# Kernel optimization log

Measured on AMD Instinct MI355X. Metric: run time of the kernel, lower is better.

## Reference

```python
import jax, jax.numpy as jnp
import numpy as np

N_NODES = 100000
N_EDGES = 1000000
IN_FEATS = 128
HID_FEATS = 128
OUT_FEATS = 128
N_CLASSES = 16
NEG_SLOPE = 0.01
BN_EPS = 1e-5


def _linear_params(key, d_in, d_out):
    k1, k2 = jax.random.split(key)
    s = 1.0 / np.sqrt(d_in)
    w = jax.random.uniform(k1, (d_in, d_out), jnp.float32, -s, s)
    b = jax.random.uniform(k2, (d_out,), jnp.float32, -s, s)
    return w, b


def setup_inputs() -> dict:
    key = jax.random.key(0)
    ks = jax.random.split(key, 16)
    node_feat = jax.random.normal(ks[0], (N_NODES, IN_FEATS), jnp.float32)
    src = jax.random.randint(ks[1], (N_EDGES,), 0, N_NODES, jnp.int32)
    dst = jax.random.randint(ks[2], (N_EDGES,), 0, N_NODES, jnp.int32)
    dims = [(IN_FEATS, HID_FEATS), (HID_FEATS, HID_FEATS), (HID_FEATS, OUT_FEATS)]
    inp = {"node_feat": node_feat, "src": src, "dst": dst}
    for i, (din, dout) in enumerate(dims):
        wp, bp = _linear_params(ks[3 + 4 * i], din, din)      # fc_pool: d_in -> d_in
        ws, _ = _linear_params(ks[4 + 4 * i], din, dout)       # fc_self (no bias)
        wn, _ = _linear_params(ks[5 + 4 * i], din, dout)       # fc_neigh (no bias)
        _, b = _linear_params(ks[6 + 4 * i], din, dout)        # shared output bias
        inp[f"wp{i}"] = wp; inp[f"bp{i}"] = bp
        inp[f"ws{i}"] = ws; inp[f"wn{i}"] = wn; inp[f"b{i}"] = b
    inp["bn_gamma"] = jnp.ones((HID_FEATS,), jnp.float32)
    inp["bn_beta"] = jnp.zeros((HID_FEATS,), jnp.float32)
    wc, bc = _linear_params(ks[15], OUT_FEATS, N_CLASSES)
    inp["wc"] = wc; inp["bc"] = bc
    return inp


def _sage_pool(h, src, dst, deg_mask, wp, bp, ws, wn, b):
    # fc_pool + relu on source nodes, gather per edge, segment-max to dst
    hp = jax.nn.relu(h @ wp + bp)                 # [N, d_in]
    msg = hp[src]                                 # [E, d_in]
    agg = jax.ops.segment_max(msg, dst, num_segments=N_NODES)  # [N, d_in]
    agg = jnp.where(deg_mask, agg, 0.0)           # zero for isolated nodes
    return h @ ws + agg @ wn + b


def _batchnorm(x, gamma, beta):
    mu = jnp.mean(x, axis=0)
    var = jnp.var(x, axis=0)
    return (x - mu) * jax.lax.rsqrt(var + BN_EPS) * gamma + beta


def reference(node_feat, src, dst,
              wp0, bp0, ws0, wn0, b0,
              wp1, bp1, ws1, wn1, b1,
              wp2, bp2, ws2, wn2, b2,
              bn_gamma, bn_beta, wc, bc):
    deg = jnp.zeros((N_NODES,), jnp.float32).at[dst].add(1.0)
    deg_mask = (deg > 0)[:, None]
    h = jax.nn.leaky_relu(_sage_pool(node_feat, src, dst, deg_mask, wp0, bp0, ws0, wn0, b0), NEG_SLOPE)
    h = jax.nn.leaky_relu(_batchnorm(_sage_pool(h, src, dst, deg_mask, wp1, bp1, ws1, wn1, b1), bn_gamma, bn_beta), NEG_SLOPE)
    h = _sage_pool(h, src, dst, deg_mask, wp2, bp2, ws2, wn2, b2)
    return h @ wc + bc
```

## Files before the change

### kernel.cpp

```cpp
#include <hip/hip_runtime.h>


#define N_NODES 100000
#define N_EDGES 1000000
#define F 128
#define NEG_SLOPE 0.01f
#define BN_EPS 1e-5f
#define NODES_PER_XCD 12500

typedef __attribute__((ext_vector_type(8))) short bf16x8;
typedef __attribute__((ext_vector_type(4))) float f32x4;
typedef __attribute__((ext_vector_type(2))) unsigned short u16x2;

typedef __attribute__((address_space(3))) unsigned int as3_uint;
typedef __attribute__((address_space(1))) const unsigned int as1_cuint;

__device__ __forceinline__ void gload16(const void* g, void* l) {
    __builtin_amdgcn_global_load_lds((as1_cuint*)g, (as3_uint*)l, 16, 0, 0);
}

__device__ __forceinline__ unsigned short f2bf(float f) {
    unsigned int u = __float_as_uint(f);
    u += 0x7fff + ((u >> 16) & 1);
    return (unsigned short)(u >> 16);
}
__device__ __forceinline__ float bf2f(unsigned short h) {
    return __uint_as_float(((unsigned int)h) << 16);
}

__global__ __launch_bounds__(256) void zero_misc_kernel(
    float4* __restrict__ deg4, float4* __restrict__ stats4)
{
    if (blockIdx.x < 98) {
        const int i = blockIdx.x * 256 + threadIdx.x;
        if (i < 25000) deg4[i] = make_float4(0.f, 0.f, 0.f, 0.f);
    } else {
        if (threadIdx.x < 64) stats4[threadIdx.x] = make_float4(0.f, 0.f, 0.f, 0.f);
    }
}

#define PREP_GROUPS 4483
__global__ __launch_bounds__(256) void prep_kernel(
    const float4* __restrict__ nf, uint2* __restrict__ xout,
    const int* __restrict__ dst, int* __restrict__ deg,
    const float* __restrict__ w0, const float* __restrict__ w1, const float* __restrict__ w2,
    const float* __restrict__ w3, const float* __restrict__ w4, const float* __restrict__ w5,
    const float* __restrict__ w6, const float* __restrict__ w7, const float* __restrict__ w8,
    short* __restrict__ wp_p, short* __restrict__ wsn_p)
{
    const int g = blockIdx.x >> 2;
    const int k = blockIdx.x & 3;
    const int tid = threadIdx.x;
    if (k < 3) {
        const int c = g * 3 + k;
        if (c >= 12500) return;
        const long i = (long)c * 256 + tid;
        float4 v = nf[i];
        uint2 o;
        o.x = (unsigned)f2bf(v.x) | ((unsigned)f2bf(v.y) << 16);
        o.y = (unsigned)f2bf(v.z) | ((unsigned)f2bf(v.w) << 16);
        xout[i] = o;
        return;
    }
    if (g < 3907) {
        const int e = g * 256 + tid;
        if (e < N_EDGES) atomicAdd(&deg[__builtin_nontemporal_load(&dst[e])], 1);
        return;
    }
    const int po = g - 3907;
    if (po >= 576) return;
    const int idx = po * 256 + tid;
    const int matid = idx >> 14;
    const int layer = (matid * 11) >> 5;
    const int mat = matid - 3 * layer;
    const int i = idx & 16383;
    const int kk = i >> 7, n = i & 127;
    const float* srcm;
    switch (matid) {
        case 0: srcm = w0; break; case 1: srcm = w1; break; case 2: srcm = w2; break;
        case 3: srcm = w3; break; case 4: srcm = w4; break; case 5: srcm = w5; break;
        case 6: srcm = w6; break; case 7: srcm = w7; break; default: srcm = w8; break;
    }
    const int slot = ((kk >> 3) * 128 + n) * 8 + (kk & 7);
    const short v = (short)f2bf(srcm[i]);
    if (mat == 0) wp_p[layer * 16384 + slot] = v;
    else wsn_p[layer * 32768 + (mat == 2 ? 16384 : 0) + slot] = v;
}

template<int NKS>
__device__ __forceinline__ void gemm_body(
    const int bid,
    const short* __restrict__ A1, const short* __restrict__ A2,
    const short* __restrict__ Bp, const float* __restrict__ bias,
    unsigned short* __restrict__ Cout, const int n_rows, const int act)
{
    constexpr int S = NKS / 2;
    __shared__ short tile[2 * 8192];

    const int tid = threadIdx.x;
    const int wave = tid >> 6;
    const int lane = tid & 63;
    const int m = lane & 15, q = lane >> 4;
    const int r0 = bid * 128;
    const int rw = (wave >> 1) * 64;
    const int r0q = r0 + rw;
    const int c0 = (wave & 1) * 64;
    const int gchunk = (tid & 7) ^ ((tid >> 3) & 7);

    f32x4 acc[4][4];
#pragma unroll
    for (int i = 0; i < 4; ++i)
#pragma unroll
        for (int j = 0; j < 4; ++j)
#pragma unroll
            for (int r = 0; r < 4; ++r) acc[i][j][r] = 0.f;

    auto stage = [&](int s, int buf) {
        const short* Ap = (NKS == 8 && s >= 2) ? A2 : A1;
        const int kbase = (s & 1) * 64;
#pragma unroll
        for (int p = 0; p < 4; ++p) {
            int row = r0 + (tid >> 3) + 32 * p;
            row = min(row, n_rows - 1);
            gload16(Ap + (size_t)row * F + kbase + gchunk * 8,
                    &tile[buf * 8192 + p * 2048 + tid * 8]);
        }
    };

    stage(0, 0);
    __syncthreads();

    for (int s = 0; s < S; ++s) {
        if (s + 1 < S) stage(s + 1, (s + 1) & 1);
        const short* tb = &tile[(s & 1) * 8192];
#pragma unroll
        for (int ks2 = 0; ks2 < 2; ++ks2) {
            const int ks32 = s * 2 + ks2;
            bf16x8 b[4], a[4];
#pragma unroll
            for (int ni = 0; ni < 4; ++ni)
                b[ni] = *(const bf16x8*)(Bp + ((size_t)(ks32 * 4 + q) * F + c0 + ni * 16 + m) * 8);
#pragma unroll
            for (int mi = 0; mi < 4; ++mi)
                a[mi] = *(const bf16x8*)(tb + (rw + mi * 16 + m) * 64 + (((ks2 * 4 + q) ^ (m & 7)) << 3));
#pragma unroll
            for (int mi = 0; mi < 4; ++mi)
#pragma unroll
                for (int ni = 0; ni < 4; ++ni)
                    acc[mi][ni] = __builtin_amdgcn_mfma_f32_16x16x32_bf16(a[mi], b[ni], acc[mi][ni], 0, 0, 0);
        }
        __syncthreads();
    }

    float bv[4];
#pragma unroll
    for (int ni = 0; ni < 4; ++ni) bv[ni] = bias[c0 + ni * 16 + m];

    short* ep = &tile[wave * 1280];
    const int colc_lo = m >> 3, cin = m & 7;
#pragma unroll
    for (int mi = 0; mi < 4; ++mi) {
#pragma unroll
        for (int ni = 0; ni < 4; ++ni) {
            const int colc = 2 * ni + colc_lo;
#pragma unroll
            for (int rg = 0; rg < 4; ++rg) {
                const int row16 = q * 4 + rg;
                float v = acc[mi][ni][rg] + bv[ni];
                if (act == 1) v = v > 0.f ? v : 0.f;
                else if (act == 2) v = v > 0.f ? v : v * NEG_SLOPE;
                ep[row16 * 80 + ((colc ^ (row16 & 7)) << 3) + cin] = (short)f2bf(v);
            }
        }
        __syncthreads();
#pragma unroll
        for (int p = 0; p < 2; ++p) {
            const int lrow = (lane >> 3) + 8 * p;
            bf16x8 vv = *(const bf16x8*)&ep[lrow * 80 + (((lane & 7) ^ (lrow & 7)) << 3)];
            const int grow = r0q + mi * 16 + lrow;
            if (grow < n_rows)
                *(bf16x8*)(Cout + (size_t)grow * F + c0 + ((lane & 7) << 3)) = vv;
        }
        __syncthreads();
    }
}

template<int NKS>
__global__ __launch_bounds__(256) void gemm_mfma(
    const short* __restrict__ A1, const short* __restrict__ A2,
    const short* __restrict__ Bp, const float* __restrict__ bias,
    unsigned short* __restrict__ Cout, int n_rows, int act)
{
    gemm_body<NKS>(blockIdx.x, A1, A2, Bp, bias, Cout, n_rows, act);
}

template<int EPI>
__global__ __launch_bounds__(256) void gemm8_fused(
    const short* __restrict__ A1, const short* __restrict__ A2,
    const short* __restrict__ Bp, const float* __restrict__ bias,
    unsigned short* __restrict__ Cout,
    const short* __restrict__ Bp2, const float* __restrict__ bias2,
    unsigned short* __restrict__ Cout2,
    float* __restrict__ stats,
    const float* __restrict__ Wc, const float* __restrict__ bc,
    float* __restrict__ out,
    int n_rows, int act)
{
    __shared__ short tile[2 * 8192];
    __shared__ float wcS[EPI == 3 ? 2064 : 4];

    const int tid = threadIdx.x;
    const int wave = tid >> 6;
    const int lane = tid & 63;
    const int m = lane & 15, q = lane >> 4;
    const int r0 = blockIdx.x * 128;
    const int rw = (wave >> 1) * 64;
    const int r0q = r0 + rw;
    const int c0 = (wave & 1) * 64;
    const int gchunk = (tid & 7) ^ ((tid >> 3) & 7);

    if constexpr (EPI == 3) {
        for (int i = tid; i < 2048; i += 256) wcS[i] = Wc[i];
        if (tid < 16) wcS[2048 + tid] = bc[tid];
    }

    f32x4 acc[4][4];
#pragma unroll
    for (int i = 0; i < 4; ++i)
#pragma unroll
        for (int j = 0; j < 4; ++j)
#pragma unroll
            for (int r = 0; r < 4; ++r) acc[i][j][r] = 0.f;

    auto stage = [&](int s, int buf) {
        const short* Ap = (s >= 2) ? A2 : A1;
        const int kbase = (s & 1) * 64;
#pragma unroll
        for (int p = 0; p < 4; ++p) {
            int row = r0 + (tid >> 3) + 32 * p;
            row = min(row, n_rows - 1);
            gload16(Ap + (size_t)row * F + kbase + gchunk * 8,
                    &tile[buf * 8192 + p * 2048 + tid * 8]);
        }
    };

    auto compute_step = [&](const short* __restrict__ Bpp, int s, f32x4 (&ac)[4][4]) {
        const short* tb = &tile[(s & 1) * 8192];
#pragma unroll
        for (int ks2 = 0; ks2 < 2; ++ks2) {
            const int ks32 = s * 2 + ks2;
            bf16x8 b[4], a[4];
#pragma unroll
            for (int ni = 0; ni < 4; ++ni)
                b[ni] = *(const bf16x8*)(Bpp + ((size_t)(ks32 * 4 + q) * F + c0 + ni * 16 + m) * 8);
#pragma unroll
            for (int mi = 0; mi < 4; ++mi)
                a[mi] = *(const bf16x8*)(tb + (rw + mi * 16 + m) * 64 + (((ks2 * 4 + q) ^ (m & 7)) << 3));
#pragma unroll
            for (int mi = 0; mi < 4; ++mi)
#pragma unroll
                for (int ni = 0; ni < 4; ++ni)
                    ac[mi][ni] = __builtin_amdgcn_mfma_f32_16x16x32_bf16(a[mi], b[ni], ac[mi][ni], 0, 0, 0);
        }
    };

    stage(0, 0);
    __syncthreads();
    for (int s = 0; s < 4; ++s) {
        if (s + 1 < 4) stage(s + 1, (s + 1) & 1);
        compute_step(Bp, s, acc);
        __syncthreads();
    }

    float bv[4];
#pragma unroll
    for (int ni = 0; ni < 4; ++ni) bv[ni] = bias[c0 + ni * 16 + m];

    if constexpr (EPI == 1 || EPI == 3) {
        const int bufo = (wave & 1) * 8192;
#pragma unroll
        for (int mi = 0; mi < 4; ++mi)
#pragma unroll
            for (int ni = 0; ni < 4; ++ni) {
                const int chunk = ni * 2 + (m >> 3);
#pragma unroll
                for (int rg = 0; rg < 4; ++rg) {
                    const int r = rw + mi * 16 + q * 4 + rg;
                    float v = acc[mi][ni][rg] + bv[ni];
                    if (act == 1) v = v > 0.f ? v : 0.f;
                    else if (act == 2) v = v > 0.f ? v : v * NEG_SLOPE;
                    tile[bufo + r * 64 + ((chunk ^ (r & 7)) << 3) + (m & 7)] = (short)f2bf(v);
                }
            }
        __syncthreads();
    }

    if constexpr (EPI == 1) {
        {
            const int r = tid >> 1, half = tid & 1;
            const int grow = r0 + r;
            if (grow < n_rows) {
#pragma unroll
                for (int c = 0; c < 8; ++c) {
                    bf16x8 vv = *(const bf16x8*)&tile[half * 8192 + r * 64 + ((c ^ (r & 7)) << 3)];
                    *(bf16x8*)(Cout + (size_t)grow * F + half * 64 + c * 8) = vv;
                }
            }
        }
        f32x4 ac2[4][4];
#pragma unroll
        for (int i = 0; i < 4; ++i)
#pragma unroll
            for (int j = 0; j < 4; ++j)
#pragma unroll
                for (int r = 0; r < 4; ++r) ac2[i][j][r] = 0.f;
        compute_step(Bp2, 0, ac2);
        compute_step(Bp2, 1, ac2);
        __syncthreads();

        float bv2[4];
#pragma unroll
        for (int ni = 0; ni < 4; ++ni) bv2[ni] = bias2[c0 + ni * 16 + m];
        short* ep = &tile[wave * 1280];
        const int colc_lo = m >> 3, cin = m & 7;
#pragma unroll
        for (int mi = 0; mi < 4; ++mi) {
#pragma unroll
            for (int ni = 0; ni < 4; ++ni) {
                const int colc = 2 * ni + colc_lo;
#pragma unroll
                for (int rg = 0; rg < 4; ++rg) {
                    const int row16 = q * 4 + rg;
                    float v = ac2[mi][ni][rg] + bv2[ni];
                    v = v > 0.f ? v : 0.f;
                    ep[row16 * 80 + ((colc ^ (row16 & 7)) << 3) + cin] = (short)f2bf(v);
                }
            }
            __syncthreads();
#pragma unroll
            for (int p = 0; p < 2; ++p) {
                const int lrow = (lane >> 3) + 8 * p;
                bf16x8 vv = *(const bf16x8*)&ep[lrow * 80 + (((lane & 7) ^ (lrow & 7)) << 3)];
                const int grow = r0q + mi * 16 + lrow;
                if (grow < n_rows)
                    *(bf16x8*)(Cout2 + (size_t)grow * F + c0 + ((lane & 7) << 3)) = vv;
            }
            __syncthreads();
        }
    }

    if constexpr (EPI == 2) {
        float* shf = (float*)&tile[8192];
        {
            float s4[4] = {0.f, 0.f, 0.f, 0.f}, ss4[4] = {0.f, 0.f, 0.f, 0.f};
#pragma unroll
            for (int mi = 0; mi < 4; ++mi)
#pragma unroll
                for (int rg = 0; rg < 4; ++rg) {
                    const int grow = r0q + mi * 16 + q * 4 + rg;
                    const bool valid = grow < n_rows;
#pragma unroll
                    for (int ni = 0; ni < 4; ++ni) {
                        float v = bf2f(f2bf(acc[mi][ni][rg] + bv[ni]));
                        if (valid) { s4[ni] += v; ss4[ni] = fmaf(v, v, ss4[ni]); }
                    }
                }
#pragma unroll
            for (int ni = 0; ni < 4; ++ni) {
                s4[ni]  += __shfl_xor(s4[ni], 16);  s4[ni]  += __shfl_xor(s4[ni], 32);
                ss4[ni] += __shfl_xor(ss4[ni], 16); ss4[ni] += __shfl_xor(ss4[ni], 32);
            }
            if (lane < 16) {
#pragma unroll
                for (int ni = 0; ni < 4; ++ni) {
                    shf[wave * 128 + m * 8 + ni * 2]     = s4[ni];
                    shf[wave * 128 + m * 8 + ni * 2 + 1] = ss4[ni];
                }
            }
        }
        short* ep = &tile[wave * 1280];
        const int colc_lo = m >> 3, cin = m & 7;
#pragma unroll
        for (int mi = 0; mi < 4; ++mi) {
#pragma unroll
            for (int ni = 0; ni < 4; ++ni) {
                const int colc = 2 * ni + colc_lo;
#pragma unroll
                for (int rg = 0; rg < 4; ++rg) {
                    const int row16 = q * 4 + rg;
                    float v = acc[mi][ni][rg] + bv[ni];
                    if (act == 1) v = v > 0.f ? v : 0.f;
                    else if (act == 2) v = v > 0.f ? v : v * NEG_SLOPE;
                    ep[row16 * 80 + ((colc ^ (row16 & 7)) << 3) + cin] = (short)f2bf(v);
                }
            }
            __syncthreads();
#pragma unroll
            for (int p = 0; p < 2; ++p) {
                const int lrow = (lane >> 3) + 8 * p;
                bf16x8 vv = *(const bf16x8*)&ep[lrow * 80 + (((lane & 7) ^ (lrow & 7)) << 3)];
                const int grow = r0q + mi * 16 + lrow;
                if (grow < n_rows)
                    *(bf16x8*)(Cout + (size_t)grow * F + c0 + ((lane & 7) << 3)) = vv;
            }
            __syncthreads();
        }
        {
            const int wp = tid >> 7, m2 = (tid >> 3) & 15, j = tid & 7;
            const float val = shf[wp * 128 + m2 * 8 + j] + shf[(wp + 2) * 128 + m2 * 8 + j];
            const int col = wp * 64 + (j >> 1) * 16 + m2;
            atomicAdd(&stats[(j & 1) * 128 + col], val);
        }
    }

    if constexpr (EPI == 3) {
        const int r = tid >> 1, cg = tid & 1;
        float sacc[8];
#pragma unroll
        for (int j = 0; j < 8; ++j) sacc[j] = wcS[2048 + cg * 8 + j];
#pragma unroll
        for (int k8 = 0; k8 < 16; ++k8) {
            const int buf = k8 >> 3, ch = k8 & 7;
            bf16x8 xa = *(const bf16x8*)&tile[buf * 8192 + r * 64 + ((ch ^ (r & 7)) << 3)];
#pragma unroll
            for (int e = 0; e < 8; ++e) {
                const float xv = bf2f((unsigned short)xa[e]);
                const float* wr = &wcS[(k8 * 8 + e) * 16 + cg * 8];
#pragma unroll
                for (int j = 0; j < 8; ++j) sacc[j] = fmaf(xv, wr[j], sacc[j]);
            }
        }
        const int grow = r0 + r;
        if (grow < n_rows) {
            float4 o0 = make_float4(sacc[0], sacc[1], sacc[2], sacc[3]);
            float4 o1 = make_float4(sacc[4], sacc[5], sacc[6], sacc[7]);
            *(float4*)(out + (size_t)grow * 16 + cg * 8) = o0;
            *(float4*)(out + (size_t)grow * 16 + cg * 8 + 4) = o1;
        }
    }
}

__global__ __launch_bounds__(256) void scan1_kernel(const int* __restrict__ deg, int* __restrict__ bsum) {
    __shared__ int sh[256];
    const int t = threadIdx.x;
    const int base = blockIdx.x * 1024 + t * 4;
    int s = 0;
#pragma unroll
    for (int j = 0; j < 4; ++j) s += (base + j < N_NODES) ? deg[base + j] : 0;
    sh[t] = s; __syncthreads();
    for (int off = 128; off; off >>= 1) {
        if (t < off) sh[t] += sh[t + off];
        __syncthreads();
    }
    if (t == 0) bsum[blockIdx.x] = sh[0];
}

__global__ __launch_bounds__(128) void scan2_kernel(int* __restrict__ bsum, int nb, int* __restrict__ row_start) {
    __shared__ int sh[128];
    const int t = threadIdx.x;
    sh[t] = (t < nb) ? bsum[t] : 0;
    __syncthreads();
    for (int off = 1; off < 128; off <<= 1) {
        int x = (t >= off) ? sh[t - off] : 0;
        __syncthreads();
        if (t >= off) sh[t] += x;
        __syncthreads();
    }
    if (t < nb) bsum[t] = t ? sh[t - 1] : 0;
    if (t == 0) row_start[N_NODES] = N_EDGES;
}

__global__ __launch_bounds__(256) void scan3_kernel(
    const int* __restrict__ deg, const int* __restrict__ boff,
    int* __restrict__ row_start, int* __restrict__ cursor)
{
    __shared__ int sh[256];
    const int t = threadIdx.x;
    const int base = blockIdx.x * 1024 + t * 4;
    int v[4]; int s = 0;
#pragma unroll
    for (int j = 0; j < 4; ++j) { v[j] = (base + j < N_NODES) ? deg[base + j] : 0; s += v[j]; }
    sh[t] = s; __syncthreads();
    for (int off = 1; off < 256; off <<= 1) {
        int x = (t >= off) ? sh[t - off] : 0;
        __syncthreads();
        if (t >= off) sh[t] += x;
        __syncthreads();
    }
    int excl = (t ? sh[t - 1] : 0) + boff[blockIdx.x];
#pragma unroll
    for (int j = 0; j < 4; ++j) {
        if (base + j < N_NODES) { row_start[base + j] = excl; cursor[base + j] = excl; }
        excl += v[j];
    }
}

__global__ __launch_bounds__(256) void scatter_gemm_kernel(
    const int* __restrict__ src, const int* __restrict__ dst,
    int* __restrict__ cursor, int* __restrict__ esrc,
    const short* __restrict__ A1, const short* __restrict__ Bp,
    const float* __restrict__ bias, unsigned short* __restrict__ Cout)
{
    const int bid = blockIdx.x;
    const int grp = bid >> 3;
    const int t8 = bid & 7;
    const int sgrp = grp / 7;
    const int u = grp - sgrp * 7;
    if (u < 5) {
        const int lo = t8 * NODES_PER_XCD;
        const int chunk = sgrp * 5 + u;
        const int e0 = chunk * 4096 + threadIdx.x;
        int d[16]; bool hit[16];
#pragma unroll
        for (int j = 0; j < 16; ++j) {
            const int e = e0 + j * 256;
            d[j] = dst[min(e, N_EDGES - 1)];
        }
#pragma unroll
        for (int j = 0; j < 16; ++j)
            hit[j] = (e0 + j * 256 < N_EDGES) & ((unsigned)(d[j] - lo) < (unsigned)NODES_PER_XCD);
        int sv[16];
#pragma unroll
        for (int j = 0; j < 16; ++j)
            if (hit[j]) sv[j] = src[e0 + j * 256];
        int pos[16];
#pragma unroll
        for (int j = 0; j < 16; ++j)
            if (hit[j]) pos[j] = atomicAdd(&cursor[d[j]], 1);
#pragma unroll
        for (int j = 0; j < 16; ++j)
            if (hit[j]) esrc[pos[j]] = sv[j];
    } else {
        const int g = (sgrp * 2 + (u - 5)) * 8 + t8;
        if (g >= (N_NODES + 127) / 128) return;
        gemm_body<4>(g, A1, (const short*)nullptr, Bp, bias, Cout, N_NODES, 1);
    }
}

__global__ __launch_bounds__(256) void aggregate_max_bf16(
    const unsigned int* __restrict__ hp, const int* __restrict__ row_start,
    const int* __restrict__ esrc, unsigned int* __restrict__ agg)
{
    const int node = blockIdx.x * 4 + (threadIdx.x >> 6);
    if (node >= N_NODES) return;
    const int lane = threadIdx.x & 63;
    const int beg = row_start[node], end = row_start[node + 1];
    u16x2 mm = (u16x2)0;
    for (int base = beg; base < end; base += 16) {
        int s[16];
#pragma unroll
        for (int j = 0; j < 16; ++j) {
            const int t = base + j;
            s[j] = esrc[(t < end) ? t : beg];
        }
        unsigned int v[16];
#pragma unroll
        for (int j = 0; j < 16; ++j) v[j] = hp[(size_t)s[j] * 64 + lane];
#pragma unroll
        for (int j = 0; j < 16; ++j)
            mm = __builtin_elementwise_max(mm, __builtin_bit_cast(u16x2, v[j]));
    }
    agg[(size_t)node * 64 + lane] = __builtin_bit_cast(unsigned int, mm);
}

__global__ void bn_finalize_kernel(
    const float* __restrict__ stats, const float* __restrict__ gamma,
    const float* __restrict__ beta, float* __restrict__ coef)
{
    const int c = threadIdx.x;
    const float mean = stats[c] * (1.f / N_NODES);
    const float var = stats[128 + c] * (1.f / N_NODES) - mean * mean;
    const float scale = gamma[c] * rsqrtf(var + BN_EPS);
    coef[c] = scale;
    coef[128 + c] = fmaf(-mean, scale, beta[c]);
}

__global__ __launch_bounds__(256) void bn_apply_bf16(
    unsigned int* __restrict__ x, const float* __restrict__ coef, long n2)
{
    __shared__ float sc[128], sf[128];
    if (threadIdx.x < 128) {
        sc[threadIdx.x] = coef[threadIdx.x];
        sf[threadIdx.x] = coef[128 + threadIdx.x];
    }
    __syncthreads();
    const long i = (long)blockIdx.x * 256 + threadIdx.x;
    if (i >= n2) return;
    const unsigned int v = x[i];
    const int c0 = (int)(i & 63) * 2;
    float a = fmaf(bf2f((unsigned short)(v & 0xffffu)), sc[c0], sf[c0]);
    float b = fmaf(bf2f((unsigned short)(v >> 16)), sc[c0 + 1], sf[c0 + 1]);
    a = a > 0.f ? a : a * NEG_SLOPE;
    b = b > 0.f ? b : b * NEG_SLOPE;
    x[i] = (unsigned)f2bf(a) | ((unsigned)f2bf(b) << 16);
}

extern "C" void kernel_launch(void* const* d_in, const int* in_sizes, int n_in,
                              void* d_out, int out_size, void* d_ws, size_t ws_size,
                              hipStream_t stream) {
    const float* node_feat = (const float*)d_in[0];
    const int* src = (const int*)d_in[1];
    const int* dst = (const int*)d_in[2];
    const float* wp[3] = {(const float*)d_in[3],  (const float*)d_in[8],  (const float*)d_in[13]};
    const float* bp[3] = {(const float*)d_in[4],  (const float*)d_in[9],  (const float*)d_in[14]};
    const float* wsm[3] = {(const float*)d_in[5], (const float*)d_in[10], (const float*)d_in[15]};
    const float* wn[3] = {(const float*)d_in[6],  (const float*)d_in[11], (const float*)d_in[16]};
    const float* bb[3] = {(const float*)d_in[7],  (const float*)d_in[12], (const float*)d_in[17]};
    const float* gamma = (const float*)d_in[18];
    const float* beta  = (const float*)d_in[19];
    const float* wc    = (const float*)d_in[20];
    const float* bc    = (const float*)d_in[21];

    const size_t SZ = (size_t)N_NODES * F;
    short* sbase = (short*)d_ws;
    short* B0  = sbase;
    short* B1  = sbase + SZ;
    short* B2  = sbase + 2 * SZ;
    short* Xbf = sbase + 3 * SZ;
    short* wp_p  = sbase + 4 * SZ;
    short* wsn_p = wp_p + 3 * 16384;
    float* fbase = (float*)(wsn_p + 3 * 32768);
    float* stats = fbase;
    float* coef  = fbase + 256;
    int* ibase = (int*)(fbase + 512);
    int* deg       = ibase;
    int* row_start = ibase + 100000;
    int* cursor    = ibase + 200104;
    int* esrc      = ibase + 300104;
    int* bsum      = ibase + 1300104;

    const int gGemm = (N_NODES + 127) / 128;
    const int gScan = (N_NODES + 1023) / 1024;
    const int gAgg  = (N_NODES + 3) / 4;
    const long n2   = (long)(SZ / 2);

    zero_misc_kernel<<<99, 256, 0, stream>>>((float4*)deg, (float4*)stats);

    prep_kernel<<<PREP_GROUPS * 4, 256, 0, stream>>>(
        (const float4*)node_feat, (uint2*)Xbf, dst, deg,
        wp[0], wsm[0], wn[0], wp[1], wsm[1], wn[1], wp[2], wsm[2], wn[2],
        wp_p, wsn_p);

    scan1_kernel<<<gScan, 256, 0, stream>>>(deg, bsum);
    scan2_kernel<<<1, 128, 0, stream>>>(bsum, gScan, row_start);
    scan3_kernel<<<gScan, 256, 0, stream>>>(deg, bsum, row_start, cursor);

    scatter_gemm_kernel<<<2744, 256, 0, stream>>>(
        src, dst, cursor, esrc,
        Xbf, wp_p, bp[0], (unsigned short*)B0);

    aggregate_max_bf16<<<gAgg, 256, 0, stream>>>(
        (const unsigned int*)B0, row_start, esrc, (unsigned int*)B1);
    gemm8_fused<1><<<gGemm, 256, 0, stream>>>(
        Xbf, B1, wsn_p, bb[0], (unsigned short*)B1,
        wp_p + 16384, bp[1], (unsigned short*)B0,
        nullptr, nullptr, nullptr, nullptr, N_NODES, 2);

    aggregate_max_bf16<<<gAgg, 256, 0, stream>>>(
        (const unsigned int*)B0, row_start, esrc, (unsigned int*)B2);
    gemm8_fused<2><<<gGemm, 256, 0, stream>>>(
        B1, B2, wsn_p + 32768, bb[1], (unsigned short*)B2,
        nullptr, nullptr, nullptr,
        stats, nullptr, nullptr, nullptr, N_NODES, 0);

    bn_finalize_kernel<<<1, 128, 0, stream>>>(stats, gamma, beta, coef);
    bn_apply_bf16<<<(int)((n2 + 255) / 256), 256, 0, stream>>>(
        (unsigned int*)B2, coef, n2);

    gemm_mfma<4><<<gGemm, 256, 0, stream>>>(B2, (const short*)nullptr,
        wp_p + 2 * 16384, bp[2], (unsigned short*)B0, N_NODES, 1);
    aggregate_max_bf16<<<gAgg, 256, 0, stream>>>(
        (const unsigned int*)B0, row_start, esrc, (unsigned int*)B1);
    gemm8_fused<3><<<gGemm, 256, 0, stream>>>(
        B2, B1, wsn_p + 2 * 32768, bb[2], nullptr,
        nullptr, nullptr, nullptr,
        nullptr, wc, bc, (float*)d_out, N_NODES, 0);
}
```

Measured before the change: 545.2 us.

## Record per-edge rank during degree count to make CSR scatter atomic-free

The degree-counting atomicAdd now stores its returned value as a 16-bit per-edge rank. The scatter step then computes each edge's slot as row_start[dst] plus that rank, so it no longer needs a cursor array or a second pass of atomics. The per-XCD partitioning of dst ranges is dropped and the scatter/GEMM block interleave is reorganised to match. The cost is one extra ushort write and read per edge, plus a random read of row_start. It also assumes no node's in-degree exceeds 65535.

```diff
diff --git a/kernel.cpp b/kernel.cpp
--- a/kernel.cpp
+++ b/kernel.cpp
@@ -6,7 +6,6 @@
 #define F 128
 #define NEG_SLOPE 0.01f
 #define BN_EPS 1e-5f
-#define NODES_PER_XCD 12500
 
 typedef __attribute__((ext_vector_type(8))) short bf16x8;
 typedef __attribute__((ext_vector_type(4))) float f32x4;
@@ -43,6 +42,7 @@
 __global__ __launch_bounds__(256) void prep_kernel(
     const float4* __restrict__ nf, uint2* __restrict__ xout,
     const int* __restrict__ dst, int* __restrict__ deg,
+    unsigned short* __restrict__ erank,
     const float* __restrict__ w0, const float* __restrict__ w1, const float* __restrict__ w2,
     const float* __restrict__ w3, const float* __restrict__ w4, const float* __restrict__ w5,
     const float* __restrict__ w6, const float* __restrict__ w7, const float* __restrict__ w8,
@@ -64,7 +64,10 @@
     }
     if (g < 3907) {
         const int e = g * 256 + tid;
-        if (e < N_EDGES) atomicAdd(&deg[__builtin_nontemporal_load(&dst[e])], 1);
+        if (e < N_EDGES) {
+            const int d = __builtin_nontemporal_load(&dst[e]);
+            erank[e] = (unsigned short)atomicAdd(&deg[d], 1);
+        }
         return;
     }
     const int po = g - 3907;
@@ -472,7 +475,7 @@
 
 __global__ __launch_bounds__(256) void scan3_kernel(
     const int* __restrict__ deg, const int* __restrict__ boff,
-    int* __restrict__ row_start, int* __restrict__ cursor)
+    int* __restrict__ row_start)
 {
     __shared__ int sh[256];
     const int t = threadIdx.x;
@@ -490,48 +493,43 @@
     int excl = (t ? sh[t - 1] : 0) + boff[blockIdx.x];
 #pragma unroll
     for (int j = 0; j < 4; ++j) {
-        if (base + j < N_NODES) { row_start[base + j] = excl; cursor[base + j] = excl; }
+        if (base + j < N_NODES) row_start[base + j] = excl;
         excl += v[j];
     }
 }
 
 __global__ __launch_bounds__(256) void scatter_gemm_kernel(
     const int* __restrict__ src, const int* __restrict__ dst,
-    int* __restrict__ cursor, int* __restrict__ esrc,
+    const unsigned short* __restrict__ erank, const int* __restrict__ row_start,
+    int* __restrict__ esrc,
     const short* __restrict__ A1, const short* __restrict__ Bp,
     const float* __restrict__ bias, unsigned short* __restrict__ Cout)
 {
     const int bid = blockIdx.x;
-    const int grp = bid >> 3;
-    const int t8 = bid & 7;
-    const int sgrp = grp / 7;
-    const int u = grp - sgrp * 7;
+    const int sgrp = bid / 13;
+    const int u = bid - sgrp * 13;
     if (u < 5) {
-        const int lo = t8 * NODES_PER_XCD;
-        const int chunk = sgrp * 5 + u;
-        const int e0 = chunk * 4096 + threadIdx.x;
-        int d[16]; bool hit[16];
-#pragma unroll
-        for (int j = 0; j < 16; ++j) {
+        const int sid = sgrp * 5 + u;
+        const int e0 = sid * 2048 + threadIdx.x;
+        if (e0 >= N_EDGES) return;
+        int d[8], sv[8]; int rk[8]; bool ok[8];
+#pragma unroll
+        for (int j = 0; j < 8; ++j) {
             const int e = e0 + j * 256;
-            d[j] = dst[min(e, N_EDGES - 1)];
-        }
-#pragma unroll
-        for (int j = 0; j < 16; ++j)
-            hit[j] = (e0 + j * 256 < N_EDGES) & ((unsigned)(d[j] - lo) < (unsigned)NODES_PER_XCD);
-        int sv[16];
-#pragma unroll
-        for (int j = 0; j < 16; ++j)
-            if (hit[j]) sv[j] = src[e0 + j * 256];
-        int pos[16];
-#pragma unroll
-        for (int j = 0; j < 16; ++j)
-            if (hit[j]) pos[j] = atomicAdd(&cursor[d[j]], 1);
-#pragma unroll
-        for (int j = 0; j < 16; ++j)
-            if (hit[j]) esrc[pos[j]] = sv[j];
+            const int ec = min(e, N_EDGES - 1);
+            ok[j] = e < N_EDGES;
+            d[j] = dst[ec];
+            sv[j] = src[ec];
+            rk[j] = erank[ec];
+        }
+        int pos[8];
+#pragma unroll
+        for (int j = 0; j < 8; ++j) pos[j] = row_start[d[j]] + rk[j];
+#pragma unroll
+        for (int j = 0; j < 8; ++j)
+            if (ok[j]) esrc[pos[j]] = sv[j];
     } else {
-        const int g = (sgrp * 2 + (u - 5)) * 8 + t8;
+        const int g = sgrp * 8 + (u - 5);
         if (g >= (N_NODES + 127) / 128) return;
         gemm_body<4>(g, A1, (const short*)nullptr, Bp, bias, Cout, N_NODES, 1);
     }
@@ -625,9 +623,9 @@
     int* ibase = (int*)(fbase + 512);
     int* deg       = ibase;
     int* row_start = ibase + 100000;
-    int* cursor    = ibase + 200104;
     int* esrc      = ibase + 300104;
     int* bsum      = ibase + 1300104;
+    unsigned short* erank = (unsigned short*)(ibase + 1300232);
 
     const int gGemm = (N_NODES + 127) / 128;
     const int gScan = (N_NODES + 1023) / 1024;
@@ -637,16 +635,16 @@
     zero_misc_kernel<<<99, 256, 0, stream>>>((float4*)deg, (float4*)stats);
 
     prep_kernel<<<PREP_GROUPS * 4, 256, 0, stream>>>(
-        (const float4*)node_feat, (uint2*)Xbf, dst, deg,
+        (const float4*)node_feat, (uint2*)Xbf, dst, deg, erank,
         wp[0], wsm[0], wn[0], wp[1], wsm[1], wn[1], wp[2], wsm[2], wn[2],
         wp_p, wsn_p);
 
     scan1_kernel<<<gScan, 256, 0, stream>>>(deg, bsum);
     scan2_kernel<<<1, 128, 0, stream>>>(bsum, gScan, row_start);
-    scan3_kernel<<<gScan, 256, 0, stream>>>(deg, bsum, row_start, cursor);
-
-    scatter_gemm_kernel<<<2744, 256, 0, stream>>>(
-        src, dst, cursor, esrc,
+    scan3_kernel<<<gScan, 256, 0, stream>>>(deg, bsum, row_start);
+
+    scatter_gemm_kernel<<<98 * 13, 256, 0, stream>>>(
+        src, dst, erank, row_start, esrc,
         Xbf, wp_p, bp[0], (unsigned short*)B0);
 
     aggregate_max_bf16<<<gAgg, 256, 0, stream>>>(
```

Result: faster. 522.4 us (-4.2%).
